# Optimization experiments

Hardware: AMD Instinct MI355X
Metric: run time of the kernel (lower is better)

The kernel has to match this reference:

```python
import jax, jax.numpy as jnp
import numpy as np

N_NODES = 100000
N_EDGES = 640000
D_IN = 128
D_OUT = 128


def setup_inputs() -> dict:
    key = jax.random.key(0)
    k1, k2, k3, k4, k5 = jax.random.split(key, 5)
    feats = jax.random.normal(k1, (N_NODES, D_IN), dtype=jnp.float32)
    src = jax.random.randint(k2, (N_EDGES,), 0, N_NODES, dtype=jnp.int32)
    dst = jax.random.randint(k3, (N_EDGES,), 0, N_NODES, dtype=jnp.int32)
    # Xavier-normal-ish init (gain for relu = sqrt(2))
    std = float(np.sqrt(2.0) * np.sqrt(2.0 / (D_IN + D_OUT)))
    linear_skip_weight = jax.random.normal(k4, (D_OUT, D_IN), dtype=jnp.float32) * std
    linear_msg_weight = jax.random.normal(k5, (D_OUT, D_IN), dtype=jnp.float32) * std
    linear_skip_bias = jnp.zeros((D_OUT,), dtype=jnp.float32)
    linear_msg_bias = jnp.zeros((D_OUT,), dtype=jnp.float32)
    return {
        "feats": feats,
        "src": src,
        "dst": dst,
        "linear_skip_weight": linear_skip_weight,
        "linear_skip_bias": linear_skip_bias,
        "linear_msg_weight": linear_msg_weight,
        "linear_msg_bias": linear_msg_bias,
    }


def reference(feats, src, dst, linear_skip_weight, linear_skip_bias,
              linear_msg_weight, linear_msg_bias):
    n = feats.shape[0]
    # degree from scatter-add of edge weights (ones) at source rows
    deg = jax.ops.segment_sum(jnp.ones_like(src, dtype=feats.dtype), src,
                              num_segments=n)
    deg_inv_sqrt = jnp.where(deg > 0, jax.lax.rsqrt(jnp.maximum(deg, 1.0)) * (deg > 0), 0.0)
    deg_inv_sqrt = jnp.where(deg > 0, deg ** -0.5, 0.0)
    # normalize source features, gather along edges, scatter-sum to dst
    feat_src = feats * deg_inv_sqrt[:, None]           # [N, D_IN]
    msgs = feat_src[src]                               # [E, D_IN]
    rst = jax.ops.segment_sum(msgs, dst, num_segments=n)  # [N, D_IN]
    rst = rst * deg_inv_sqrt[:, None]
    rst_ = rst @ linear_msg_weight.T + linear_msg_bias
    skip_x = feats @ linear_skip_weight.T + linear_skip_bias
    return rst_ + skip_x
```

## Files before the change

kernel.cpp:

```cpp
#include <hip/hip_runtime.h>

#define N_NODES 100000
#define N_EDGES 640000
#define D 128
#define NB ((N_NODES + 1023) / 1024)
#define BKT_C 16
#define OVF_CAP 32768

typedef short v8s __attribute__((ext_vector_type(8)));
typedef float v4f __attribute__((ext_vector_type(4)));

__device__ __forceinline__ unsigned short f2bf(float x) {
    unsigned int u = __builtin_bit_cast(unsigned int, x);
    u += 0x7fffu + ((u >> 16) & 1u);
    return (unsigned short)(u >> 16);
}
__device__ __forceinline__ float bf2f(unsigned int hi) {
    return __builtin_bit_cast(float, hi << 16);
}

__global__ __launch_bounds__(256) void k_zero(int4* __restrict__ pk4,
                                              int* __restrict__ ovf_cnt) {
    int i = blockIdx.x * blockDim.x + threadIdx.x;
    if (i < N_NODES / 4) pk4[i] = make_int4(0, 0, 0, 0);
    if (i == 0) *ovf_cnt = 0;
}

__global__ __launch_bounds__(256) void k_pre(const float* __restrict__ feats,
                                             const float* __restrict__ Wm,
                                             const float* __restrict__ Ws,
                                             const float* __restrict__ bmsg,
                                             const float* __restrict__ bskip,
                                             const int* __restrict__ src,
                                             const int* __restrict__ dst,
                                             unsigned int* __restrict__ pk,
                                             unsigned short* __restrict__ Bcat,
                                             float* __restrict__ bias,
                                             char* __restrict__ outb,
                                             int* __restrict__ bucket,
                                             int* __restrict__ ovf_cnt,
                                             int2* __restrict__ ovf) {
    int i = blockIdx.x * blockDim.x + threadIdx.x;
    if (i < D * D) {
        int j = i >> 7;
        int k = i & 127;
        Bcat[j * 256 + k]       = f2bf(Wm[i]);
        Bcat[j * 256 + 128 + k] = f2bf(Ws[i]);
    }
    if (i < D) bias[i] = bmsg[i] + bskip[i];
    if (i < N_EDGES) {
        int s = src[i];
        int d = dst[i];
        atomicAdd(&pk[s], 1u);
        unsigned int old = atomicAdd(&pk[d], 0x10000u);
        if (bucket) {
            unsigned int p = old >> 16;
            if (p < BKT_C) {
                bucket[d * BKT_C + (int)p] = s;
            } else {
                int q = atomicAdd(ovf_cnt, 1);
                if (q < OVF_CAP) ovf[q] = make_int2(d, s);
            }
        }
    }
    int g = i * 8;
    int row = g >> 7;
    int col = g & 127;
    if (row < N_NODES) {
        const float4* sp = (const float4*)(feats + g);
        float4 x = sp[0], y = sp[1];
        uint4 p;
        p.x = (unsigned)f2bf(x.x) | ((unsigned)f2bf(x.y) << 16);
        p.y = (unsigned)f2bf(x.z) | ((unsigned)f2bf(x.w) << 16);
        p.z = (unsigned)f2bf(y.x) | ((unsigned)f2bf(y.y) << 16);
        p.w = (unsigned)f2bf(y.z) | ((unsigned)f2bf(y.w) << 16);
        *(uint4*)(outb + (size_t)row * 512 + 256 + col * 2) = p;
    }
}

__global__ __launch_bounds__(256) void k_scan1(const unsigned int* __restrict__ pk,
                                               int* __restrict__ rowptr,
                                               int* __restrict__ bsums) {
    __shared__ int sd[256];
    int t = threadIdx.x;
    int i0 = blockIdx.x * 1024 + t * 4;
    int v[4];
    int s = 0;
#pragma unroll
    for (int q = 0; q < 4; q++) {
        int i = i0 + q;
        v[q] = (i < N_NODES) ? (int)(pk[i] >> 16) : 0;
        s += v[q];
    }
    sd[t] = s;
    __syncthreads();
    for (int off = 1; off < 256; off <<= 1) {
        int y = (t >= off) ? sd[t - off] : 0;
        __syncthreads();
        sd[t] += y;
        __syncthreads();
    }
    int run = sd[t] - s;
    if (t == 255) bsums[blockIdx.x] = sd[255];
#pragma unroll
    for (int q = 0; q < 4; q++) {
        int i = i0 + q;
        if (i < N_NODES) rowptr[i] = run;
        run += v[q];
    }
}

__global__ __launch_bounds__(128) void k_scan2(int* __restrict__ bsums) {
    __shared__ int sd[128];
    int t = threadIdx.x;
    int v = (t < NB) ? bsums[t] : 0;
    sd[t] = v;
    __syncthreads();
    for (int off = 1; off < 128; off <<= 1) {
        int y = (t >= off) ? sd[t - off] : 0;
        __syncthreads();
        sd[t] += y;
        __syncthreads();
    }
    if (t < NB) bsums[t] = sd[t] - v;
}

__global__ __launch_bounds__(256) void k_scan3(const int* __restrict__ bsums,
                                               int* __restrict__ rowptr) {
    int add = bsums[blockIdx.x];
    int i0 = blockIdx.x * 1024 + threadIdx.x * 4;
#pragma unroll
    for (int q = 0; q < 4; q++) {
        int i = i0 + q;
        if (i < N_NODES) rowptr[i] += add;
    }
}

__global__ __launch_bounds__(256) void k_fill(const int* __restrict__ src,
                                              const int* __restrict__ dst,
                                              int* __restrict__ rowptr,
                                              int* __restrict__ csr_src) {
    int e = blockIdx.x * blockDim.x + threadIdx.x;
    if (e < N_EDGES) {
        int p = atomicAdd(&rowptr[dst[e]], 1);
        csr_src[p] = src[e];
    }
}

__device__ __forceinline__ void agg_edge(const char* outb,
                                         const unsigned int* pk,
                                         int s, int sub, float* acc) {
    float sc = rsqrtf((float)(pk[s] & 0xffffu));
    uint4 v = *(const uint4*)(outb + (size_t)s * 512 + 256 + sub * 16);
    acc[0] += bf2f(v.x & 0xffffu) * sc;
    acc[1] += bf2f(v.x >> 16) * sc;
    acc[2] += bf2f(v.y & 0xffffu) * sc;
    acc[3] += bf2f(v.y >> 16) * sc;
    acc[4] += bf2f(v.z & 0xffffu) * sc;
    acc[5] += bf2f(v.z >> 16) * sc;
    acc[6] += bf2f(v.w & 0xffffu) * sc;
    acc[7] += bf2f(v.w >> 16) * sc;
}

__device__ __forceinline__ void agg_acc(uint4 v, float sc, float* acc) {
    acc[0] += bf2f(v.x & 0xffffu) * sc;
    acc[1] += bf2f(v.x >> 16) * sc;
    acc[2] += bf2f(v.y & 0xffffu) * sc;
    acc[3] += bf2f(v.y >> 16) * sc;
    acc[4] += bf2f(v.z & 0xffffu) * sc;
    acc[5] += bf2f(v.z >> 16) * sc;
    acc[6] += bf2f(v.w & 0xffffu) * sc;
    acc[7] += bf2f(v.w >> 16) * sc;
}

__device__ __forceinline__ void agg_finish(char* outb, int wid,
                                           unsigned int pkn, int grp, int sub,
                                           float* acc) {
#pragma unroll
    for (int i = 0; i < 8; i++) {
        acc[i] += __shfl_xor(acc[i], 16);
        acc[i] += __shfl_xor(acc[i], 32);
    }
    if (grp == 0) {
        int dsrc = (int)(pkn & 0xffffu);
        float scn = (dsrc > 0) ? rsqrtf((float)dsrc) : 0.0f;
        uint4 p;
        p.x = (unsigned)f2bf(acc[0] * scn) | ((unsigned)f2bf(acc[1] * scn) << 16);
        p.y = (unsigned)f2bf(acc[2] * scn) | ((unsigned)f2bf(acc[3] * scn) << 16);
        p.z = (unsigned)f2bf(acc[4] * scn) | ((unsigned)f2bf(acc[5] * scn) << 16);
        p.w = (unsigned)f2bf(acc[6] * scn) | ((unsigned)f2bf(acc[7] * scn) << 16);
        *(uint4*)(outb + (size_t)wid * 512 + sub * 16) = p;
    }
}

__global__ __launch_bounds__(256) void k_agg_bkt(char* __restrict__ outb,
                                                 const unsigned int* __restrict__ pk,
                                                 const int* __restrict__ bucket,
                                                 const int* __restrict__ ovf_cnt,
                                                 const int2* __restrict__ ovf) {
    int wid = (int)((blockIdx.x * (unsigned)blockDim.x + threadIdx.x) >> 6);
    int lane = threadIdx.x & 63;
    if (wid >= N_NODES) return;
    int grp = lane >> 4;
    int sub = lane & 15;
    unsigned int pkn = pk[wid];
    int cnt = (int)(pkn >> 16);
    int m = cnt < BKT_C ? cnt : BKT_C;
    const int* bk = bucket + wid * BKT_C;

    int4 bq = *(const int4*)(bk + grp * 4);
    int e0 = grp * 4;

    bool a0 = e0 < m, a1 = e0 + 1 < m, a2 = e0 + 2 < m, a3 = e0 + 3 < m;
    int sA = a0 ? bq.x : 0; float gA = a0 ? 1.0f : 0.0f;
    int sB = a1 ? bq.y : 0; float gB = a1 ? 1.0f : 0.0f;
    int sC = a2 ? bq.z : 0; float gC = a2 ? 1.0f : 0.0f;
    int sD = a3 ? bq.w : 0; float gD = a3 ? 1.0f : 0.0f;

    unsigned int pA = pk[sA];
    unsigned int pB = pk[sB];
    unsigned int pC = pk[sC];
    unsigned int pD = pk[sD];
    uint4 vA = *(const uint4*)(outb + (size_t)sA * 512 + 256 + sub * 16);
    uint4 vB = *(const uint4*)(outb + (size_t)sB * 512 + 256 + sub * 16);
    uint4 vC = *(const uint4*)(outb + (size_t)sC * 512 + 256 + sub * 16);
    uint4 vD = *(const uint4*)(outb + (size_t)sD * 512 + 256 + sub * 16);

    float scA = gA * rsqrtf(fmaxf((float)(pA & 0xffffu), 1.0f));
    float scB = gB * rsqrtf(fmaxf((float)(pB & 0xffffu), 1.0f));
    float scC = gC * rsqrtf(fmaxf((float)(pC & 0xffffu), 1.0f));
    float scD = gD * rsqrtf(fmaxf((float)(pD & 0xffffu), 1.0f));

    float acc[8];
#pragma unroll
    for (int i = 0; i < 8; i++) acc[i] = 0.f;
    agg_acc(vA, scA, acc);
    agg_acc(vB, scB, acc);
    agg_acc(vC, scC, acc);
    agg_acc(vD, scD, acc);

    if (cnt > BKT_C) {
        int no = *ovf_cnt;
        if (no > OVF_CAP) no = OVF_CAP;
        for (int i = grp; i < no; i += 4) {
            int2 p = ovf[i];
            if (p.x == wid) agg_edge(outb, pk, p.y, sub, acc);
        }
    }
    agg_finish(outb, wid, pkn, grp, sub, acc);
}

__global__ __launch_bounds__(256) void k_agg_csr(char* __restrict__ outb,
                                                 const unsigned int* __restrict__ pk,
                                                 const int* __restrict__ rowptr,
                                                 const int* __restrict__ csr_src) {
    int wid = (int)((blockIdx.x * (unsigned)blockDim.x + threadIdx.x) >> 6);
    int lane = threadIdx.x & 63;
    if (wid >= N_NODES) return;
    int grp = lane >> 4;
    int sub = lane & 15;
    int start = (wid == 0) ? 0 : rowptr[wid - 1];
    int end = rowptr[wid];
    float acc[8];
#pragma unroll
    for (int i = 0; i < 8; i++) acc[i] = 0.f;
    for (int base = start; base < end; base += 4) {
        int e = base + grp;
        if (e < end) agg_edge(outb, pk, csr_src[e], sub, acc);
    }
    agg_finish(outb, wid, pk[wid], grp, sub, acc);
}

__global__ __launch_bounds__(256) void k_gemm(const unsigned short* __restrict__ Bcat,
                                              const float* __restrict__ bias,
                                              float* __restrict__ outf) {
    __shared__ unsigned short Bl[128][264];
    const char* Ab = (const char*)outf;
    int tid = threadIdx.x;
    int lane = tid & 63;
    int w = tid >> 6;
    int n0 = blockIdx.x * 128;

    for (int i = tid; i < 128 * 32; i += 256) {
        int r = i >> 5, c = i & 31;
        *(uint4*)(&Bl[r][c * 8]) = *(const uint4*)(Bcat + r * 256 + c * 8);
    }
    __syncthreads();

    int q = lane >> 4;
    int lr = lane & 15;

    int r0 = n0 + w * 32 + lr;      if (r0 > N_NODES - 1) r0 = N_NODES - 1;
    int r1 = n0 + w * 32 + 16 + lr; if (r1 > N_NODES - 1) r1 = N_NODES - 1;
    const char* a0p = Ab + (size_t)r0 * 512 + q * 16;
    const char* a1p = Ab + (size_t)r1 * 512 + q * 16;

    v4f acc[2][8];
#pragma unroll
    for (int mt = 0; mt < 2; mt++)
#pragma unroll
        for (int t = 0; t < 8; t++) acc[mt][t] = (v4f){0.f, 0.f, 0.f, 0.f};

#pragma unroll
    for (int kk = 0; kk < 8; kk++) {
        v8s a0 = *(const v8s*)(a0p + kk * 64);
        v8s a1 = *(const v8s*)(a1p + kk * 64);
#pragma unroll
        for (int t = 0; t < 8; t++) {
            v8s b = *(const v8s*)(&Bl[t * 16 + lr][kk * 32 + q * 8]);
            acc[0][t] = __builtin_amdgcn_mfma_f32_16x16x32_bf16(a0, b, acc[0][t], 0, 0, 0);
            acc[1][t] = __builtin_amdgcn_mfma_f32_16x16x32_bf16(a1, b, acc[1][t], 0, 0, 0);
        }
    }

#pragma unroll
    for (int t = 0; t < 8; t++) {
        float bv = bias[t * 16 + lr];
#pragma unroll
        for (int mt = 0; mt < 2; mt++) {
            int rowb = n0 + w * 32 + mt * 16 + q * 4;
#pragma unroll
            for (int r = 0; r < 4; r++) {
                int row = rowb + r;
                if (row < N_NODES)
                    outf[(size_t)row * 128 + t * 16 + lr] = acc[mt][t][r] + bv;
            }
        }
    }
}

extern "C" void kernel_launch(void* const* d_in, const int* in_sizes, int n_in,
                              void* d_out, int out_size, void* d_ws, size_t ws_size,
                              hipStream_t stream) {
    const float* feats = (const float*)d_in[0];
    const int*   src   = (const int*)d_in[1];
    const int*   dst   = (const int*)d_in[2];
    const float* Wskip = (const float*)d_in[3];
    const float* bskip = (const float*)d_in[4];
    const float* Wmsg  = (const float*)d_in[5];
    const float* bmsg  = (const float*)d_in[6];

    char* w = (char*)d_ws;

    bool pathA = ws_size >= (size_t)7128320;

    if (pathA) {
        unsigned int*   pk      = (unsigned int*)w;
        int*            ovf_cnt = (int*)(w + 400000);
        unsigned short* Bcat    = (unsigned short*)(w + 400128);
        float*          bias    = (float*)(w + 465664);
        int*            bucket  = (int*)(w + 466176);
        int2*           ovf     = (int2*)(w + 6866176);

        hipLaunchKernelGGL(k_zero, dim3((N_NODES / 4 + 255) / 256), dim3(256), 0,
                           stream, (int4*)pk, ovf_cnt);
        hipLaunchKernelGGL(k_pre, dim3((N_NODES * (D / 8) + 255) / 256), dim3(256),
                           0, stream, feats, Wmsg, Wskip, bmsg, bskip, src, dst, pk,
                           Bcat, bias, (char*)d_out, bucket, ovf_cnt, ovf);
        hipLaunchKernelGGL(k_agg_bkt, dim3((N_NODES * 64 + 255) / 256), dim3(256), 0,
                           stream, (char*)d_out, pk, bucket, ovf_cnt, ovf);
        hipLaunchKernelGGL(k_gemm, dim3((N_NODES + 127) / 128), dim3(256), 0, stream,
                           Bcat, bias, (float*)d_out);
    } else {
        unsigned int*   pk      = (unsigned int*)w;
        int*            rowptr  = (int*)(w + 400000);
        int*            bsums   = (int*)(w + 800128);
        unsigned short* Bcat    = (unsigned short*)(w + 800640);
        float*          bias    = (float*)(w + 866176);
        int*            csr_src = (int*)(w + 866688);

        hipLaunchKernelGGL(k_zero, dim3((N_NODES / 4 + 255) / 256), dim3(256), 0,
                           stream, (int4*)pk, (int*)(w + 400000) );
        hipLaunchKernelGGL(k_pre, dim3((N_NODES * (D / 8) + 255) / 256), dim3(256),
                           0, stream, feats, Wmsg, Wskip, bmsg, bskip, src, dst, pk,
                           Bcat, bias, (char*)d_out, (int*)nullptr, (int*)nullptr,
                           (int2*)nullptr);
        hipLaunchKernelGGL(k_scan1, dim3(NB), dim3(256), 0, stream, pk, rowptr,
                           bsums);
        hipLaunchKernelGGL(k_scan2, dim3(1), dim3(128), 0, stream, bsums);
        hipLaunchKernelGGL(k_scan3, dim3(NB), dim3(256), 0, stream, bsums, rowptr);
        hipLaunchKernelGGL(k_fill, dim3((N_EDGES + 255) / 256), dim3(256), 0, stream,
                           src, dst, rowptr, csr_src);
        hipLaunchKernelGGL(k_agg_csr, dim3((N_NODES * 64 + 255) / 256), dim3(256), 0,
                           stream, (char*)d_out, pk, rowptr, csr_src);
        hipLaunchKernelGGL(k_gemm, dim3((N_NODES + 127) / 128), dim3(256), 0, stream,
                           Bcat, bias, (float*)d_out);
    }
}
```

Measured before the change: 234.6 us.

## Fuse neighbor aggregation into the MFMA GEMM kernel via an LDS tile

```diff
diff --git a/kernel.cpp b/kernel.cpp
--- a/kernel.cpp
+++ b/kernel.cpp
@@ -78,6 +78,149 @@
     }
 }
 
+__global__ __launch_bounds__(256) void k_fused(const float* __restrict__ feats,
+                                               const unsigned int* __restrict__ pk,
+                                               const int* __restrict__ bucket,
+                                               const int* __restrict__ ovf_cnt,
+                                               const int2* __restrict__ ovf,
+                                               const unsigned short* __restrict__ Bcat,
+                                               const float* __restrict__ bias,
+                                               float* __restrict__ outf) {
+    __shared__ unsigned short aggh[128][132];
+    int tid = threadIdx.x;
+    int lane = tid & 63;
+    int w = tid >> 6;
+    int n0 = blockIdx.x * 128;
+    int grp = lane >> 4;
+    int sub = lane & 15;
+
+#pragma unroll 2
+    for (int j = 0; j < 32; ++j) {
+        int wid = n0 + w * 32 + j;
+        int widc = wid < N_NODES ? wid : N_NODES - 1;
+        unsigned int pkn = pk[widc];
+        int cnt = (int)(pkn >> 16);
+        int m = cnt < BKT_C ? cnt : BKT_C;
+        const int* bk = bucket + widc * BKT_C;
+
+        int4 bq = *(const int4*)(bk + grp * 4);
+        int e0 = grp * 4;
+        bool a0 = e0 < m, a1 = e0 + 1 < m, a2 = e0 + 2 < m, a3 = e0 + 3 < m;
+        int sA = a0 ? bq.x : 0; float gA = a0 ? 1.0f : 0.0f;
+        int sB = a1 ? bq.y : 0; float gB = a1 ? 1.0f : 0.0f;
+        int sC = a2 ? bq.z : 0; float gC = a2 ? 1.0f : 0.0f;
+        int sD = a3 ? bq.w : 0; float gD = a3 ? 1.0f : 0.0f;
+
+        unsigned int pA = pk[sA];
+        unsigned int pB = pk[sB];
+        unsigned int pC = pk[sC];
+        unsigned int pD = pk[sD];
+        const float4* rA = (const float4*)(feats + (size_t)sA * 128 + sub * 8);
+        const float4* rB = (const float4*)(feats + (size_t)sB * 128 + sub * 8);
+        const float4* rC = (const float4*)(feats + (size_t)sC * 128 + sub * 8);
+        const float4* rD = (const float4*)(feats + (size_t)sD * 128 + sub * 8);
+        float4 uA = rA[0], vA = rA[1];
+        float4 uB = rB[0], vB = rB[1];
+        float4 uC = rC[0], vC = rC[1];
+        float4 uD = rD[0], vD = rD[1];
+
+        float scA = gA * rsqrtf(fmaxf((float)(pA & 0xffffu), 1.0f));
+        float scB = gB * rsqrtf(fmaxf((float)(pB & 0xffffu), 1.0f));
+        float scC = gC * rsqrtf(fmaxf((float)(pC & 0xffffu), 1.0f));
+        float scD = gD * rsqrtf(fmaxf((float)(pD & 0xffffu), 1.0f));
+
+        float acc[8];
+#pragma unroll
+        for (int i = 0; i < 8; i++) acc[i] = 0.f;
+        acc[0] += uA.x * scA; acc[1] += uA.y * scA; acc[2] += uA.z * scA; acc[3] += uA.w * scA;
+        acc[4] += vA.x * scA; acc[5] += vA.y * scA; acc[6] += vA.z * scA; acc[7] += vA.w * scA;
+        acc[0] += uB.x * scB; acc[1] += uB.y * scB; acc[2] += uB.z * scB; acc[3] += uB.w * scB;
+        acc[4] += vB.x * scB; acc[5] += vB.y * scB; acc[6] += vB.z * scB; acc[7] += vB.w * scB;
+        acc[0] += uC.x * scC; acc[1] += uC.y * scC; acc[2] += uC.z * scC; acc[3] += uC.w * scC;
+        acc[4] += vC.x * scC; acc[5] += vC.y * scC; acc[6] += vC.z * scC; acc[7] += vC.w * scC;
+        acc[0] += uD.x * scD; acc[1] += uD.y * scD; acc[2] += uD.z * scD; acc[3] += uD.w * scD;
+        acc[4] += vD.x * scD; acc[5] += vD.y * scD; acc[6] += vD.z * scD; acc[7] += vD.w * scD;
+
+        if (cnt > BKT_C) {
+            int no = *ovf_cnt;
+            if (no > OVF_CAP) no = OVF_CAP;
+            for (int i = grp; i < no; i += 4) {
+                int2 p = ovf[i];
+                if (p.x == widc) {
+                    float sc = rsqrtf((float)(pk[p.y] & 0xffffu));
+                    const float4* rp = (const float4*)(feats + (size_t)p.y * 128 + sub * 8);
+                    float4 u = rp[0], v = rp[1];
+                    acc[0] += u.x * sc; acc[1] += u.y * sc; acc[2] += u.z * sc; acc[3] += u.w * sc;
+                    acc[4] += v.x * sc; acc[5] += v.y * sc; acc[6] += v.z * sc; acc[7] += v.w * sc;
+                }
+            }
+        }
+
+#pragma unroll
+        for (int i = 0; i < 8; i++) {
+            acc[i] += __shfl_xor(acc[i], 16);
+            acc[i] += __shfl_xor(acc[i], 32);
+        }
+        if (grp == 0) {
+            int dsrc = (int)(pkn & 0xffffu);
+            float scn = (dsrc > 0) ? rsqrtf((float)dsrc) : 0.0f;
+            uint4 p;
+            p.x = (unsigned)f2bf(acc[0] * scn) | ((unsigned)f2bf(acc[1] * scn) << 16);
+            p.y = (unsigned)f2bf(acc[2] * scn) | ((unsigned)f2bf(acc[3] * scn) << 16);
+            p.z = (unsigned)f2bf(acc[4] * scn) | ((unsigned)f2bf(acc[5] * scn) << 16);
+            p.w = (unsigned)f2bf(acc[6] * scn) | ((unsigned)f2bf(acc[7] * scn) << 16);
+            *(uint4*)(&aggh[w * 32 + j][sub * 8]) = p;
+        }
+    }
+
+    const char* Ab = (const char*)outf;
+    int q = grp;
+    int lr = sub;
+    int r0 = n0 + w * 32 + lr;      int r0c = r0 < N_NODES ? r0 : N_NODES - 1;
+    int r1 = r0 + 16;               int r1c = r1 < N_NODES ? r1 : N_NODES - 1;
+    const char* a0p = Ab + (size_t)r0c * 512 + 256 + q * 16;
+    const char* a1p = Ab + (size_t)r1c * 512 + 256 + q * 16;
+
+    v4f acc2[2][8];
+#pragma unroll
+    for (int mt = 0; mt < 2; mt++)
+#pragma unroll
+        for (int t = 0; t < 8; t++) acc2[mt][t] = (v4f){0.f, 0.f, 0.f, 0.f};
+
+#pragma unroll
+    for (int kk = 0; kk < 8; kk++) {
+        v8s a0, a1;
+        if (kk < 4) {
+            a0 = *(const v8s*)(&aggh[w * 32 + lr][q * 8 + kk * 32]);
+            a1 = *(const v8s*)(&aggh[w * 32 + 16 + lr][q * 8 + kk * 32]);
+        } else {
+            a0 = *(const v8s*)(a0p + (kk - 4) * 64);
+            a1 = *(const v8s*)(a1p + (kk - 4) * 64);
+        }
+#pragma unroll
+        for (int t = 0; t < 8; t++) {
+            v8s b = *(const v8s*)(Bcat + (t * 16 + lr) * 256 + kk * 32 + q * 8);
+            acc2[0][t] = __builtin_amdgcn_mfma_f32_16x16x32_bf16(a0, b, acc2[0][t], 0, 0, 0);
+            acc2[1][t] = __builtin_amdgcn_mfma_f32_16x16x32_bf16(a1, b, acc2[1][t], 0, 0, 0);
+        }
+    }
+
+#pragma unroll
+    for (int t = 0; t < 8; t++) {
+        float bv = bias[t * 16 + lr];
+#pragma unroll
+        for (int mt = 0; mt < 2; mt++) {
+            int rowb = n0 + w * 32 + mt * 16 + q * 4;
+#pragma unroll
+            for (int r = 0; r < 4; r++) {
+                int row = rowb + r;
+                if (row < N_NODES)
+                    outf[(size_t)row * 128 + t * 16 + lr] = acc2[mt][t][r] + bv;
+            }
+        }
+    }
+}
+
 __global__ __launch_bounds__(256) void k_scan1(const unsigned int* __restrict__ pk,
                                                int* __restrict__ rowptr,
                                                int* __restrict__ bsums) {
@@ -162,17 +305,6 @@
     acc[7] += bf2f(v.w >> 16) * sc;
 }
 
-__device__ __forceinline__ void agg_acc(uint4 v, float sc, float* acc) {
-    acc[0] += bf2f(v.x & 0xffffu) * sc;
-    acc[1] += bf2f(v.x >> 16) * sc;
-    acc[2] += bf2f(v.y & 0xffffu) * sc;
-    acc[3] += bf2f(v.y >> 16) * sc;
-    acc[4] += bf2f(v.z & 0xffffu) * sc;
-    acc[5] += bf2f(v.z >> 16) * sc;
-    acc[6] += bf2f(v.w & 0xffffu) * sc;
-    acc[7] += bf2f(v.w >> 16) * sc;
-}
-
 __device__ __forceinline__ void agg_finish(char* outb, int wid,
                                            unsigned int pkn, int grp, int sub,
                                            float* acc) {
@@ -191,63 +323,6 @@
         p.w = (unsigned)f2bf(acc[6] * scn) | ((unsigned)f2bf(acc[7] * scn) << 16);
         *(uint4*)(outb + (size_t)wid * 512 + sub * 16) = p;
     }
-}
-
-__global__ __launch_bounds__(256) void k_agg_bkt(char* __restrict__ outb,
-                                                 const unsigned int* __restrict__ pk,
-                                                 const int* __restrict__ bucket,
-                                                 const int* __restrict__ ovf_cnt,
-                                                 const int2* __restrict__ ovf) {
-    int wid = (int)((blockIdx.x * (unsigned)blockDim.x + threadIdx.x) >> 6);
-    int lane = threadIdx.x & 63;
-    if (wid >= N_NODES) return;
-    int grp = lane >> 4;
-    int sub = lane & 15;
-    unsigned int pkn = pk[wid];
-    int cnt = (int)(pkn >> 16);
-    int m = cnt < BKT_C ? cnt : BKT_C;
-    const int* bk = bucket + wid * BKT_C;
-
-    int4 bq = *(const int4*)(bk + grp * 4);
-    int e0 = grp * 4;
-
-    bool a0 = e0 < m, a1 = e0 + 1 < m, a2 = e0 + 2 < m, a3 = e0 + 3 < m;
-    int sA = a0 ? bq.x : 0; float gA = a0 ? 1.0f : 0.0f;
-    int sB = a1 ? bq.y : 0; float gB = a1 ? 1.0f : 0.0f;
-    int sC = a2 ? bq.z : 0; float gC = a2 ? 1.0f : 0.0f;
-    int sD = a3 ? bq.w : 0; float gD = a3 ? 1.0f : 0.0f;
-
-    unsigned int pA = pk[sA];
-    unsigned int pB = pk[sB];
-    unsigned int pC = pk[sC];
-    unsigned int pD = pk[sD];
-    uint4 vA = *(const uint4*)(outb + (size_t)sA * 512 + 256 + sub * 16);
-    uint4 vB = *(const uint4*)(outb + (size_t)sB * 512 + 256 + sub * 16);
-    uint4 vC = *(const uint4*)(outb + (size_t)sC * 512 + 256 + sub * 16);
-    uint4 vD = *(const uint4*)(outb + (size_t)sD * 512 + 256 + sub * 16);
-
-    float scA = gA * rsqrtf(fmaxf((float)(pA & 0xffffu), 1.0f));
-    float scB = gB * rsqrtf(fmaxf((float)(pB & 0xffffu), 1.0f));
-    float scC = gC * rsqrtf(fmaxf((float)(pC & 0xffffu), 1.0f));
-    float scD = gD * rsqrtf(fmaxf((float)(pD & 0xffffu), 1.0f));
-
-    float acc[8];
-#pragma unroll
-    for (int i = 0; i < 8; i++) acc[i] = 0.f;
-    agg_acc(vA, scA, acc);
-    agg_acc(vB, scB, acc);
-    agg_acc(vC, scC, acc);
-    agg_acc(vD, scD, acc);
-
-    if (cnt > BKT_C) {
-        int no = *ovf_cnt;
-        if (no > OVF_CAP) no = OVF_CAP;
-        for (int i = grp; i < no; i += 4) {
-            int2 p = ovf[i];
-            if (p.x == wid) agg_edge(outb, pk, p.y, sub, acc);
-        }
-    }
-    agg_finish(outb, wid, pkn, grp, sub, acc);
 }
 
 __global__ __launch_bounds__(256) void k_agg_csr(char* __restrict__ outb,
@@ -357,10 +432,9 @@
         hipLaunchKernelGGL(k_pre, dim3((N_NODES * (D / 8) + 255) / 256), dim3(256),
                            0, stream, feats, Wmsg, Wskip, bmsg, bskip, src, dst, pk,
                            Bcat, bias, (char*)d_out, bucket, ovf_cnt, ovf);
-        hipLaunchKernelGGL(k_agg_bkt, dim3((N_NODES * 64 + 255) / 256), dim3(256), 0,
-                           stream, (char*)d_out, pk, bucket, ovf_cnt, ovf);
-        hipLaunchKernelGGL(k_gemm, dim3((N_NODES + 127) / 128), dim3(256), 0, stream,
-                           Bcat, bias, (float*)d_out);
+        hipLaunchKernelGGL(k_fused, dim3((N_NODES + 127) / 128), dim3(256), 0,
+                           stream, feats, pk, bucket, ovf_cnt, ovf, Bcat, bias,
+                           (float*)d_out);
     } else {
         unsigned int*   pk      = (unsigned int*)w;
         int*            rowptr  = (int*)(w + 400000);
```

New measurement: 283.1 us. 20.7% more time.
